# Kernel tuning notes

Hardware: AMD Instinct MI355X
Metric: run time of the kernel (lower is better)

## Reference

```python
import jax, jax.numpy as jnp
import numpy as np

N_NODES = 100000


def gcn_conv(x, W, b, src, dst, n):
    # PyG GCNConv: linear transform, add self-loops, symmetric degree normalization,
    # scatter-add aggregation from src -> dst, then bias.
    h = x @ W  # [N, F_out]
    loop = jnp.arange(n, dtype=src.dtype)
    s = jnp.concatenate([src, loop])  # sources incl. self-loops
    d = jnp.concatenate([dst, loop])  # targets incl. self-loops
    deg = jax.ops.segment_sum(jnp.ones_like(d, dtype=h.dtype), d, num_segments=n)
    dinv = jnp.where(deg > 0, jax.lax.rsqrt(deg), 0.0)
    norm = dinv[s] * dinv[d]  # [E+N]
    msg = h[s] * norm[:, None]  # gather + scale
    out = jax.ops.segment_sum(msg, d, num_segments=n)  # scatter-add
    return out + b


def setup_inputs() -> dict:
    key = jax.random.key(0)
    k1, k2, k3, k4 = jax.random.split(key, 4)
    n, e = N_NODES, 1600000
    z = jax.random.normal(k1, (n, 64), dtype=jnp.float32)
    edge_index = jax.random.randint(k2, (2, e), 0, n, dtype=jnp.int64)
    # Glorot-ish init for weights, zero bias (PyG default bias init is zeros)
    W1 = jax.random.normal(k3, (64, 128), dtype=jnp.float32) * (1.0 / np.sqrt(64))
    b1 = jnp.zeros((128,), dtype=jnp.float32)
    W2 = jax.random.normal(k4, (128, 64), dtype=jnp.float32) * (1.0 / np.sqrt(128))
    b2 = jnp.zeros((64,), dtype=jnp.float32)
    return {"z": z, "edge_index": edge_index, "W1": W1, "b1": b1, "W2": W2, "b2": b2}


def reference(z, edge_index, W1, b1, W2, b2):
    n = z.shape[0]
    src, dst = edge_index[0], edge_index[1]
    h = gcn_conv(z, W1, b1, src, dst, n)
    h = jax.nn.relu(h)
    x_hat = gcn_conv(h, W2, b2, src, dst, n)
    return x_hat
```

## Files before the change

kernel.cpp:

```cpp
#include <hip/hip_runtime.h>
#include <hip/hip_bf16.h>


#define WAVE 64
#define BSHIFT 8
#define NPB 256
#define CAP 5120
#define CH 4096
#define NBMAX 512

__device__ inline float bf16_to_f32(unsigned short h) {
    return __uint_as_float(((unsigned int)h) << 16);
}
__device__ inline unsigned short f32_to_bf16(float f) {
    unsigned int x = __float_as_uint(f);
    return (unsigned short)((x + 0x7FFFu + ((x >> 16) & 1u)) >> 16);
}

__global__ void zero_i32(int* __restrict__ p, int n) {
    int i = blockIdx.x * blockDim.x + threadIdx.x;
    if (i < n) p[i] = 0;
}

__global__ __launch_bounds__(256) void bin_edges(
        const int* __restrict__ src, const int* __restrict__ dst,
        int* __restrict__ bcursor, int2* __restrict__ ebuf, int E, int NB)
{
    __shared__ int hist[NBMAX];
    __shared__ int cur[NBMAX];
    const int t  = threadIdx.x;
    const int e0 = blockIdx.x * CH;

    for (int b = t; b < NB; b += 256) hist[b] = 0;
    __syncthreads();

#pragma unroll
    for (int j = 0; j < CH / 256; ++j) {
        int e = e0 + j * 256 + t;
        if (e < E) atomicAdd(&hist[dst[e] >> BSHIFT], 1);
    }
    __syncthreads();

    for (int b = t; b < NB; b += 256) {
        int c = hist[b];
        cur[b] = (c > 0) ? atomicAdd(&bcursor[b], c) : 0;
    }
    __syncthreads();

#pragma unroll
    for (int j = 0; j < CH / 256; ++j) {
        int e = e0 + j * 256 + t;
        if (e < E) {
            int s = src[e], d = dst[e];
            int b = d >> BSHIFT;
            int pos = atomicAdd(&cur[b], 1);
            ebuf[(size_t)b * CAP + pos] = make_int2(s, d);
        }
    }
}

__global__ __launch_bounds__(256) void build_csr(
        const int2* __restrict__ ebuf, const int* __restrict__ bcursor,
        float* __restrict__ dinv, int* __restrict__ rbeg, int* __restrict__ rend,
        int* __restrict__ csr, int N)
{
    __shared__ int h[NPB];
    __shared__ int tmp[NPB];
    const int t   = threadIdx.x;
    const int b   = blockIdx.x;
    const int n0  = b << BSHIFT;
    const int cnt = bcursor[b];
    const size_t base = (size_t)b * CAP;

    h[t] = 0;
    __syncthreads();

    for (int i = t; i < cnt; i += 256)
        atomicAdd(&h[ebuf[base + i].y - n0], 1);
    __syncthreads();

    int deg = h[t];
    tmp[t] = deg;
    __syncthreads();
    for (int off = 1; off < 256; off <<= 1) {
        int x = (t >= off) ? tmp[t - off] : 0;
        __syncthreads();
        tmp[t] += x;
        __syncthreads();
    }
    int st = tmp[t] - deg;

    int node = n0 + t;
    if (node < N) {
        dinv[node] = rsqrtf((float)deg + 1.0f);
        rbeg[node] = (int)base + st;
        rend[node] = (int)base + st + deg;
    }
    h[t] = st;
    __syncthreads();

    for (int i = t; i < cnt; i += 256) {
        int2 e = ebuf[base + i];
        int p = atomicAdd(&h[e.y - n0], 1);
        csr[base + p] = e.x;
    }
}

__global__ void scale_to_bf16(const float* __restrict__ z, const float* __restrict__ dinv,
                              unsigned short* __restrict__ u, int N)
{
    int i = blockIdx.x * blockDim.x + threadIdx.x;
    if (i >= N * 16) return;
    float di = dinv[i >> 4];
    float4 v = ((const float4*)z)[i];
    ushort4 o;
    o.x = f32_to_bf16(v.x * di);
    o.y = f32_to_bf16(v.y * di);
    o.z = f32_to_bf16(v.z * di);
    o.w = f32_to_bf16(v.w * di);
    ((ushort4*)u)[i] = o;
}

template<int K, int F, int ROWS, bool ADD_BIAS, bool RELU, bool BF16_OUT>
__global__ __launch_bounds__(256) void gemm_fused(
        const float* __restrict__ A, const float* __restrict__ W,
        const float* __restrict__ dinv, const float* __restrict__ b,
        void* __restrict__ out_, int N)
{
    constexpr int C4  = F / 4;
    constexpr int G   = 256 / C4;
    constexpr int RPT = ROWS / G;
    constexpr int KQ  = K / 4;
    constexpr int AST = KQ + 1;
    __shared__ float4 Wl[K * C4];
    __shared__ float4 Al[ROWS * AST];

    const int tid  = threadIdx.x;
    const int row0 = blockIdx.x * ROWS;

    for (int i = tid; i < K * C4; i += 256) Wl[i] = ((const float4*)W)[i];
    for (int i = tid; i < ROWS * KQ; i += 256) {
        int r = i / KQ, kq = i % KQ;
        int gr = row0 + r;
        float4 v = make_float4(0.f, 0.f, 0.f, 0.f);
        if (gr < N) v = ((const float4*)(A + (size_t)gr * K))[kq];
        Al[r * AST + kq] = v;
    }
    __syncthreads();

    const int c4 = tid % C4;
    const int rg = tid / C4;

    float4 acc[RPT];
#pragma unroll
    for (int r = 0; r < RPT; ++r) acc[r] = make_float4(0.f, 0.f, 0.f, 0.f);

#pragma unroll 2
    for (int kq = 0; kq < KQ; ++kq) {
        float4 w0 = Wl[(4 * kq + 0) * C4 + c4];
        float4 w1 = Wl[(4 * kq + 1) * C4 + c4];
        float4 w2 = Wl[(4 * kq + 2) * C4 + c4];
        float4 w3 = Wl[(4 * kq + 3) * C4 + c4];
#pragma unroll
        for (int r = 0; r < RPT; ++r) {
            float4 a = Al[(rg * RPT + r) * AST + kq];
            acc[r].x += a.x * w0.x; acc[r].y += a.x * w0.y;
            acc[r].z += a.x * w0.z; acc[r].w += a.x * w0.w;
            acc[r].x += a.y * w1.x; acc[r].y += a.y * w1.y;
            acc[r].z += a.y * w1.z; acc[r].w += a.y * w1.w;
            acc[r].x += a.z * w2.x; acc[r].y += a.z * w2.y;
            acc[r].z += a.z * w2.z; acc[r].w += a.z * w2.w;
            acc[r].x += a.w * w3.x; acc[r].y += a.w * w3.y;
            acc[r].z += a.w * w3.z; acc[r].w += a.w * w3.w;
        }
    }

#pragma unroll
    for (int r = 0; r < RPT; ++r) {
        int gr = row0 + rg * RPT + r;
        if (gr < N) {
            float di = dinv[gr];
            float4 o = acc[r];
            o.x *= di; o.y *= di; o.z *= di; o.w *= di;
            if (ADD_BIAS) {
                float4 bb = ((const float4*)b)[c4];
                o.x += bb.x; o.y += bb.y; o.z += bb.z; o.w += bb.w;
            }
            if (RELU) {
                o.x = fmaxf(o.x, 0.0f); o.y = fmaxf(o.y, 0.0f);
                o.z = fmaxf(o.z, 0.0f); o.w = fmaxf(o.w, 0.0f);
            }
            if (BF16_OUT) {
                ushort4 ob;
                ob.x = f32_to_bf16(o.x); ob.y = f32_to_bf16(o.y);
                ob.z = f32_to_bf16(o.z); ob.w = f32_to_bf16(o.w);
                ((ushort4*)((unsigned short*)out_ + (size_t)gr * F))[c4] = ob;
            } else {
                ((float4*)((float*)out_ + (size_t)gr * F))[c4] = o;
            }
        }
    }
}

template<bool POST>
__global__ __launch_bounds__(256) void aggregate64_bf16(
        const unsigned short* __restrict__ hs, const int* __restrict__ rbeg,
        const int* __restrict__ rend, const int* __restrict__ csr,
        const float* __restrict__ dinv, const float* __restrict__ b,
        float* __restrict__ out, int N)
{
    int node = (int)((blockIdx.x * (size_t)blockDim.x + threadIdx.x) >> 6);
    int lane = threadIdx.x & 63;
    if (node >= N) return;
    node = __builtin_amdgcn_readfirstlane(node);

    const int beg = rbeg[node];
    const int end = rend[node];

    float acc = bf16_to_f32(hs[(size_t)node * 64 + lane]);

    int e = beg;
    for (; e + 16 <= end; e += 16) {
        int s[16];
#pragma unroll
        for (int j = 0; j < 16; ++j) s[j] = csr[e + j];
        float v[16];
#pragma unroll
        for (int j = 0; j < 16; ++j) v[j] = bf16_to_f32(hs[(size_t)s[j] * 64 + lane]);
        float t0 = ((v[0] + v[1]) + (v[2] + v[3])) + ((v[4] + v[5]) + (v[6] + v[7]));
        float t1 = ((v[8] + v[9]) + (v[10] + v[11])) + ((v[12] + v[13]) + (v[14] + v[15]));
        acc += t0 + t1;
    }
    for (; e + 4 <= end; e += 4) {
        int s0 = csr[e+0], s1 = csr[e+1], s2 = csr[e+2], s3 = csr[e+3];
        float v0 = bf16_to_f32(hs[(size_t)s0 * 64 + lane]);
        float v1 = bf16_to_f32(hs[(size_t)s1 * 64 + lane]);
        float v2 = bf16_to_f32(hs[(size_t)s2 * 64 + lane]);
        float v3 = bf16_to_f32(hs[(size_t)s3 * 64 + lane]);
        acc += (v0 + v1) + (v2 + v3);
    }
    for (; e < end; ++e)
        acc += bf16_to_f32(hs[(size_t)csr[e] * 64 + lane]);

    float o = acc;
    if (POST) o = dinv[node] * acc + b[lane];
    out[(size_t)node * 64 + lane] = o;
}

static inline size_t align_up(size_t x, size_t a) { return (x + a - 1) / a * a; }

extern "C" void kernel_launch(void* const* d_in, const int* in_sizes, int n_in,
                              void* d_out, int out_size, void* d_ws, size_t ws_size,
                              hipStream_t stream) {
    const float* z    = (const float*)d_in[0];
    const int*   eidx = (const int*)d_in[1];
    const float* W1   = (const float*)d_in[2];
    const float* b1   = (const float*)d_in[3];
    const float* W2   = (const float*)d_in[4];
    const float* b2   = (const float*)d_in[5];
    float* out = (float*)d_out;

    const int N = in_sizes[0] / 64;
    const int E = in_sizes[1] / 2;
    const int* src = eidx;
    const int* dst = eidx + E;
    const int NB = (N + NPB - 1) >> BSHIFT;

    char* ws = (char*)d_ws;
    size_t off = 0;
    float* dinv    = (float*)(ws + off); off = align_up(off + (size_t)N * 4, 512);
    int*   rbeg    = (int*)  (ws + off); off = align_up(off + (size_t)N * 4, 512);
    int*   rend    = (int*)  (ws + off); off = align_up(off + (size_t)N * 4, 512);
    int*   bcursor = (int*)  (ws + off); off = align_up(off + (size_t)NBMAX * 4, 512);
    int*   csr     = (int*)  (ws + off); off = align_up(off + (size_t)NB * CAP * 4, 512);
    float* bufA    = (float*)(ws + off); off = align_up(off + (size_t)N * 64 * 4, 512);
    float* bufB    = (float*)(ws + off); off = align_up(off + (size_t)N * 64 * 4, 512);
    float* bufC    = (float*)(ws + off); off = align_up(off + (size_t)N * 128 * 4, 512);
    int2*  ebuf    = (int2*)bufC;
    (void)ws_size;

    unsigned short* u    = (unsigned short*)bufA;
    float*          agg1 = bufB;
    float*          x1   = bufC;
    unsigned short* hs2  = (unsigned short*)bufA;

    zero_i32<<<(NB + 255) / 256, 256, 0, stream>>>(bcursor, NB);
    bin_edges<<<(E + CH - 1) / CH, 256, 0, stream>>>(src, dst, bcursor, ebuf, E, NB);
    build_csr<<<NB, 256, 0, stream>>>(ebuf, bcursor, dinv, rbeg, rend, csr, N);

    scale_to_bf16<<<((size_t)N * 16 + 255) / 256, 256, 0, stream>>>(z, dinv, u, N);
    aggregate64_bf16<false><<<(N + 3) / 4, 256, 0, stream>>>(u, rbeg, rend, csr, dinv, nullptr, agg1, N);
    constexpr int ROWS = 64;
    gemm_fused<64, 128, ROWS, true, true, false><<<(N + ROWS - 1) / ROWS, 256, 0, stream>>>(
        agg1, W1, dinv, b1, x1, N);

    gemm_fused<128, 64, ROWS, false, false, true><<<(N + ROWS - 1) / ROWS, 256, 0, stream>>>(
        x1, W2, dinv, nullptr, hs2, N);
    aggregate64_bf16<true><<<(N + 3) / 4, 256, 0, stream>>>(hs2, rbeg, rend, csr, dinv, b2, out, N);
}
```

Baseline: 280.9 us.

## Fuse both GEMMs into one kernel and fold bf16 scaling into CSR build

Merges the two dense layer transforms into a single kernel that keeps the 128-wide hidden activations in shared memory, so x1 is never written to or read back from global memory. The kernel reloads W2 into the same shared buffer between stages and uses a smaller 32-row tile. It also moves the dinv-scaled bf16 conversion of z into the end of build_csr, which removes one launch and a reread of dinv. The costs are larger shared-memory use per block, lower occupancy, an extra weight reload per block, and more serial work inside build_csr.

```diff
diff --git a/kernel.cpp b/kernel.cpp
--- a/kernel.cpp
+++ b/kernel.cpp
@@ -61,11 +61,13 @@
 
 __global__ __launch_bounds__(256) void build_csr(
         const int2* __restrict__ ebuf, const int* __restrict__ bcursor,
-        float* __restrict__ dinv, int* __restrict__ rbeg, int* __restrict__ rend,
-        int* __restrict__ csr, int N)
+        const float* __restrict__ z, float* __restrict__ dinv,
+        int* __restrict__ rbeg, int* __restrict__ rend,
+        int* __restrict__ csr, unsigned short* __restrict__ u, int N)
 {
-    __shared__ int h[NPB];
-    __shared__ int tmp[NPB];
+    __shared__ int   h[NPB];
+    __shared__ int   tmp[NPB];
+    __shared__ float sdv[NPB];
     const int t   = threadIdx.x;
     const int b   = blockIdx.x;
     const int n0  = b << BSHIFT;
@@ -91,8 +93,10 @@
     int st = tmp[t] - deg;
 
     int node = n0 + t;
+    float di = rsqrtf((float)deg + 1.0f);
+    sdv[t] = di;
     if (node < N) {
-        dinv[node] = rsqrtf((float)deg + 1.0f);
+        dinv[node] = di;
         rbeg[node] = (int)base + st;
         rend[node] = (int)base + st + deg;
     }
@@ -104,101 +108,18 @@
         int p = atomicAdd(&h[e.y - n0], 1);
         csr[base + p] = e.x;
     }
-}
-
-__global__ void scale_to_bf16(const float* __restrict__ z, const float* __restrict__ dinv,
-                              unsigned short* __restrict__ u, int N)
-{
-    int i = blockIdx.x * blockDim.x + threadIdx.x;
-    if (i >= N * 16) return;
-    float di = dinv[i >> 4];
-    float4 v = ((const float4*)z)[i];
-    ushort4 o;
-    o.x = f32_to_bf16(v.x * di);
-    o.y = f32_to_bf16(v.y * di);
-    o.z = f32_to_bf16(v.z * di);
-    o.w = f32_to_bf16(v.w * di);
-    ((ushort4*)u)[i] = o;
-}
-
-template<int K, int F, int ROWS, bool ADD_BIAS, bool RELU, bool BF16_OUT>
-__global__ __launch_bounds__(256) void gemm_fused(
-        const float* __restrict__ A, const float* __restrict__ W,
-        const float* __restrict__ dinv, const float* __restrict__ b,
-        void* __restrict__ out_, int N)
-{
-    constexpr int C4  = F / 4;
-    constexpr int G   = 256 / C4;
-    constexpr int RPT = ROWS / G;
-    constexpr int KQ  = K / 4;
-    constexpr int AST = KQ + 1;
-    __shared__ float4 Wl[K * C4];
-    __shared__ float4 Al[ROWS * AST];
-
-    const int tid  = threadIdx.x;
-    const int row0 = blockIdx.x * ROWS;
-
-    for (int i = tid; i < K * C4; i += 256) Wl[i] = ((const float4*)W)[i];
-    for (int i = tid; i < ROWS * KQ; i += 256) {
-        int r = i / KQ, kq = i % KQ;
-        int gr = row0 + r;
-        float4 v = make_float4(0.f, 0.f, 0.f, 0.f);
-        if (gr < N) v = ((const float4*)(A + (size_t)gr * K))[kq];
-        Al[r * AST + kq] = v;
-    }
-    __syncthreads();
-
-    const int c4 = tid % C4;
-    const int rg = tid / C4;
-
-    float4 acc[RPT];
-#pragma unroll
-    for (int r = 0; r < RPT; ++r) acc[r] = make_float4(0.f, 0.f, 0.f, 0.f);
-
-#pragma unroll 2
-    for (int kq = 0; kq < KQ; ++kq) {
-        float4 w0 = Wl[(4 * kq + 0) * C4 + c4];
-        float4 w1 = Wl[(4 * kq + 1) * C4 + c4];
-        float4 w2 = Wl[(4 * kq + 2) * C4 + c4];
-        float4 w3 = Wl[(4 * kq + 3) * C4 + c4];
-#pragma unroll
-        for (int r = 0; r < RPT; ++r) {
-            float4 a = Al[(rg * RPT + r) * AST + kq];
-            acc[r].x += a.x * w0.x; acc[r].y += a.x * w0.y;
-            acc[r].z += a.x * w0.z; acc[r].w += a.x * w0.w;
-            acc[r].x += a.y * w1.x; acc[r].y += a.y * w1.y;
-            acc[r].z += a.y * w1.z; acc[r].w += a.y * w1.w;
-            acc[r].x += a.z * w2.x; acc[r].y += a.z * w2.y;
-            acc[r].z += a.z * w2.z; acc[r].w += a.z * w2.w;
-            acc[r].x += a.w * w3.x; acc[r].y += a.w * w3.y;
-            acc[r].z += a.w * w3.z; acc[r].w += a.w * w3.w;
-        }
-    }
-
-#pragma unroll
-    for (int r = 0; r < RPT; ++r) {
-        int gr = row0 + rg * RPT + r;
-        if (gr < N) {
-            float di = dinv[gr];
-            float4 o = acc[r];
-            o.x *= di; o.y *= di; o.z *= di; o.w *= di;
-            if (ADD_BIAS) {
-                float4 bb = ((const float4*)b)[c4];
-                o.x += bb.x; o.y += bb.y; o.z += bb.z; o.w += bb.w;
-            }
-            if (RELU) {
-                o.x = fmaxf(o.x, 0.0f); o.y = fmaxf(o.y, 0.0f);
-                o.z = fmaxf(o.z, 0.0f); o.w = fmaxf(o.w, 0.0f);
-            }
-            if (BF16_OUT) {
-                ushort4 ob;
-                ob.x = f32_to_bf16(o.x); ob.y = f32_to_bf16(o.y);
-                ob.z = f32_to_bf16(o.z); ob.w = f32_to_bf16(o.w);
-                ((ushort4*)((unsigned short*)out_ + (size_t)gr * F))[c4] = ob;
-            } else {
-                ((float4*)((float*)out_ + (size_t)gr * F))[c4] = o;
-            }
-        }
+
+    const int nloc = (N - n0 < NPB) ? (N - n0) : NPB;
+    for (int i = t; i < nloc * 16; i += 256) {
+        int r = i >> 4, kq = i & 15;
+        float d2 = sdv[r];
+        float4 v = ((const float4*)(z + (size_t)(n0 + r) * 64))[kq];
+        ushort4 o;
+        o.x = f32_to_bf16(v.x * d2);
+        o.y = f32_to_bf16(v.y * d2);
+        o.z = f32_to_bf16(v.z * d2);
+        o.w = f32_to_bf16(v.w * d2);
+        ((ushort4*)(u + (size_t)(n0 + r) * 64))[kq] = o;
     }
 }
 
@@ -245,6 +166,128 @@
     float o = acc;
     if (POST) o = dinv[node] * acc + b[lane];
     out[(size_t)node * 64 + lane] = o;
+}
+
+#define TILE 32
+__global__ __launch_bounds__(256) void gemm12(
+        const float* __restrict__ agg1, const float* __restrict__ W1,
+        const float* __restrict__ b1, const float* __restrict__ W2,
+        const float* __restrict__ dinv, unsigned short* __restrict__ hs2, int N)
+{
+    __shared__ float4 Wl[2048];
+    __shared__ float4 Al[TILE * 17];
+    __shared__ float4 X1[TILE * 33];
+    __shared__ float  sdv[TILE];
+
+    const int tid  = threadIdx.x;
+    const int row0 = blockIdx.x * TILE;
+
+#pragma unroll
+    for (int i = tid; i < 2048; i += 256) Wl[i] = ((const float4*)W1)[i];
+    for (int i = tid; i < TILE * 16; i += 256) {
+        int r = i >> 4, kq = i & 15;
+        int gr = row0 + r;
+        float4 v = make_float4(0.f, 0.f, 0.f, 0.f);
+        if (gr < N) v = ((const float4*)(agg1 + (size_t)gr * 64))[kq];
+        Al[r * 17 + kq] = v;
+    }
+    if (tid < TILE) {
+        int gr = row0 + tid;
+        sdv[tid] = (gr < N) ? dinv[gr] : 0.0f;
+    }
+    __syncthreads();
+
+    {
+        constexpr int C4 = 32, G = 8, RPT = TILE / G;
+        const int c4 = tid % C4;
+        const int rg = tid / C4;
+        float4 acc[RPT];
+#pragma unroll
+        for (int r = 0; r < RPT; ++r) acc[r] = make_float4(0.f, 0.f, 0.f, 0.f);
+
+#pragma unroll 2
+        for (int kq = 0; kq < 16; ++kq) {
+            float4 w0 = Wl[(4 * kq + 0) * C4 + c4];
+            float4 w1 = Wl[(4 * kq + 1) * C4 + c4];
+            float4 w2 = Wl[(4 * kq + 2) * C4 + c4];
+            float4 w3 = Wl[(4 * kq + 3) * C4 + c4];
+#pragma unroll
+            for (int r = 0; r < RPT; ++r) {
+                float4 a = Al[(rg * RPT + r) * 17 + kq];
+                acc[r].x += a.x * w0.x; acc[r].y += a.x * w0.y;
+                acc[r].z += a.x * w0.z; acc[r].w += a.x * w0.w;
+                acc[r].x += a.y * w1.x; acc[r].y += a.y * w1.y;
+                acc[r].z += a.y * w1.z; acc[r].w += a.y * w1.w;
+                acc[r].x += a.z * w2.x; acc[r].y += a.z * w2.y;
+                acc[r].z += a.z * w2.z; acc[r].w += a.z * w2.w;
+                acc[r].x += a.w * w3.x; acc[r].y += a.w * w3.y;
+                acc[r].z += a.w * w3.z; acc[r].w += a.w * w3.w;
+            }
+        }
+
+        float4 bb = ((const float4*)b1)[c4];
+#pragma unroll
+        for (int r = 0; r < RPT; ++r) {
+            int lr = rg * RPT + r;
+            float di = sdv[lr];
+            float4 o = acc[r];
+            o.x = fmaxf(o.x * di + bb.x, 0.0f);
+            o.y = fmaxf(o.y * di + bb.y, 0.0f);
+            o.z = fmaxf(o.z * di + bb.z, 0.0f);
+            o.w = fmaxf(o.w * di + bb.w, 0.0f);
+            X1[lr * 33 + c4] = o;
+        }
+    }
+    __syncthreads();
+
+#pragma unroll
+    for (int i = tid; i < 2048; i += 256) Wl[i] = ((const float4*)W2)[i];
+    __syncthreads();
+
+    {
+        constexpr int C4 = 16, G = 16, RPT = TILE / G;
+        const int c4 = tid % C4;
+        const int rg = tid / C4;
+        float4 acc[RPT];
+#pragma unroll
+        for (int r = 0; r < RPT; ++r) acc[r] = make_float4(0.f, 0.f, 0.f, 0.f);
+
+#pragma unroll 2
+        for (int kq = 0; kq < 32; ++kq) {
+            float4 w0 = Wl[(4 * kq + 0) * C4 + c4];
+            float4 w1 = Wl[(4 * kq + 1) * C4 + c4];
+            float4 w2 = Wl[(4 * kq + 2) * C4 + c4];
+            float4 w3 = Wl[(4 * kq + 3) * C4 + c4];
+#pragma unroll
+            for (int r = 0; r < RPT; ++r) {
+                float4 a = X1[(rg * RPT + r) * 33 + kq];
+                acc[r].x += a.x * w0.x; acc[r].y += a.x * w0.y;
+                acc[r].z += a.x * w0.z; acc[r].w += a.x * w0.w;
+                acc[r].x += a.y * w1.x; acc[r].y += a.y * w1.y;
+                acc[r].z += a.y * w1.z; acc[r].w += a.y * w1.w;
+                acc[r].x += a.z * w2.x; acc[r].y += a.z * w2.y;
+                acc[r].z += a.z * w2.z; acc[r].w += a.z * w2.w;
+                acc[r].x += a.w * w3.x; acc[r].y += a.w * w3.y;
+                acc[r].z += a.w * w3.z; acc[r].w += a.w * w3.w;
+            }
+        }
+
+#pragma unroll
+        for (int r = 0; r < RPT; ++r) {
+            int lr = rg * RPT + r;
+            int gr = row0 + lr;
+            if (gr < N) {
+                float di = sdv[lr];
+                float4 o = acc[r];
+                ushort4 ob;
+                ob.x = f32_to_bf16(o.x * di);
+                ob.y = f32_to_bf16(o.y * di);
+                ob.z = f32_to_bf16(o.z * di);
+                ob.w = f32_to_bf16(o.w * di);
+                ((ushort4*)(hs2 + (size_t)gr * 64))[c4] = ob;
+            }
+        }
+    }
 }
 
 static inline size_t align_up(size_t x, size_t a) { return (x + a - 1) / a * a; }
@@ -281,20 +324,15 @@
 
     unsigned short* u    = (unsigned short*)bufA;
     float*          agg1 = bufB;
-    float*          x1   = bufC;
     unsigned short* hs2  = (unsigned short*)bufA;
 
     zero_i32<<<(NB + 255) / 256, 256, 0, stream>>>(bcursor, NB);
     bin_edges<<<(E + CH - 1) / CH, 256, 0, stream>>>(src, dst, bcursor, ebuf, E, NB);
-    build_csr<<<NB, 256, 0, stream>>>(ebuf, bcursor, dinv, rbeg, rend, csr, N);
-
-    scale_to_bf16<<<((size_t)N * 16 + 255) / 256, 256, 0, stream>>>(z, dinv, u, N);
+    build_csr<<<NB, 256, 0, stream>>>(ebuf, bcursor, z, dinv, rbeg, rend, csr, u, N);
+
     aggregate64_bf16<false><<<(N + 3) / 4, 256, 0, stream>>>(u, rbeg, rend, csr, dinv, nullptr, agg1, N);
-    constexpr int ROWS = 64;
-    gemm_fused<64, 128, ROWS, true, true, false><<<(N + ROWS - 1) / ROWS, 256, 0, stream>>>(
-        agg1, W1, dinv, b1, x1, N);
-
-    gemm_fused<128, 64, ROWS, false, false, true><<<(N + ROWS - 1) / ROWS, 256, 0, stream>>>(
-        x1, W2, dinv, nullptr, hs2, N);
+
+    gemm12<<<(N + TILE - 1) / TILE, 256, 0, stream>>>(agg1, W1, b1, W2, dinv, hs2, N);
+
     aggregate64_bf16<true><<<(N + 3) / 4, 256, 0, stream>>>(hs2, rbeg, rend, csr, dinv, b2, out, N);
 }
```

After: 276.4 us. About the same (-1.6%).
